# Performance work log

Measured on AMD Instinct MI355X. Metric: run time of the kernel, lower is better.

## Reference

```python
import jax, jax.numpy as jnp
import numpy as np

# Production-scale dims: N tokens = 64 batch x 8192 seq, hidden width 256.
N, D_IN, D_OUT = 524288, 256, 256
P_NONZERO = 0.05  # mimics bnn.random.calc_desired_var -> sparse ternary W


def binarise(v):
    # bnn.functions.binarise forward: sign with binarise(0) = +1
    return jnp.where(v >= 0, 1.0, -1.0).astype(v.dtype)


def setup_inputs() -> dict:
    key = jax.random.key(0)
    kx, kw = jax.random.split(key)
    # x: binary activations in {-1,+1} (output of a previous binarise layer)
    x = jnp.where(jax.random.normal(kx, (N, D_IN)) >= 0, 1.0, -1.0).astype(jnp.float32)
    # W: ternary {-1, 0, +1} with Var = P_NONZERO (values +-1 each w.p. p/2)
    u = jax.random.uniform(kw, (D_IN, D_OUT))
    W = jnp.where(u < P_NONZERO / 2, -1.0,
                  jnp.where(u < P_NONZERO, 1.0, 0.0)).astype(jnp.float32)
    return {"x": x, "W": W}


def reference(x, W):
    # integer = x @ W  (ternary-weight matmul; int math in torch, same values in fp32)
    integer = x @ W  # [N, D_OUT]
    return binarise(integer)
```

## Files before the change

kernel.cpp:

```cpp
#include <hip/hip_runtime.h>
#include <stdint.h>


#define NROWS 524288
#define DDIM  256
#define BLOCKS 2048
#define ROWS_PER_BLOCK (NROWS / BLOCKS)

typedef uint32_t u32;
typedef unsigned long long u64;

#define LOADG(v0, v1, v2, v3, ptr)                                   \
    v0 = *reinterpret_cast<const uint4*>(ptr);                       \
    v1 = *reinterpret_cast<const uint4*>((ptr) + DDIM);              \
    v2 = *reinterpret_cast<const uint4*>((ptr) + 2 * DDIM);          \
    v3 = *reinterpret_cast<const uint4*>((ptr) + 3 * DDIM);

#define PROC1(xv, optr)                                               \
    {                                                                 \
        const u64 _bl0 = __ballot((int)(xv).x < 0);                   \
        const u64 _bl1 = __ballot((int)(xv).y < 0);                   \
        const u64 _bl2 = __ballot((int)(xv).z < 0);                   \
        const u64 _bl3 = __ballot((int)(xv).w < 0);                   \
        int _p = 0;                                                   \
        _p += __popc(((u32)_bl0         ^ M0) & A0);                  \
        _p += __popc(((u32)(_bl0 >> 32) ^ M1) & A1);                  \
        _p += __popc(((u32)_bl1         ^ M2) & A2);                  \
        _p += __popc(((u32)(_bl1 >> 32) ^ M3) & A3);                  \
        _p += __popc(((u32)_bl2         ^ M4) & A4);                  \
        _p += __popc(((u32)(_bl2 >> 32) ^ M5) & A5);                  \
        _p += __popc(((u32)_bl3         ^ M6) & A6);                  \
        _p += __popc(((u32)(_bl3 >> 32) ^ M7) & A7);                  \
        const int _d = C - 2 * _p;                                    \
        const u32 _o = 0x3f800000u | ((u32)_d & 0x80000000u);         \
        __builtin_nontemporal_store(_o, reinterpret_cast<u32*>(optr));\
    }

#define PROC4(v0, v1, v2, v3, optr)                                  \
    PROC1(v0, (optr));                                               \
    PROC1(v1, (optr) + DDIM);                                        \
    PROC1(v2, (optr) + 2 * DDIM);                                    \
    PROC1(v3, (optr) + 3 * DDIM);

__global__ __launch_bounds__(256, 4)
void ternbin_kernel(const float* __restrict__ x, const float* __restrict__ W,
                    float* __restrict__ out) {
    const int t    = threadIdx.x;
    const int lane = t & 63;
    const int wv   = t >> 6;
    const int col  = (wv << 6) | lane;

    u32 A0=0,A1=0,A2=0,A3=0,A4=0,A5=0,A6=0,A7=0;
    u32 M0=0,M1=0,M2=0,M3=0,M4=0,M5=0,M6=0,M7=0;
    #pragma unroll 8
    for (int k = 0; k < DDIM; ++k) {
        const float v = W[k * DDIM + col];
        const int   w = ((k & 3) << 1) | (k >> 7);
        const u32 bit = 1u << ((k >> 2) & 31);
        const u32 nz  = (v != 0.0f) ? bit : 0u;
        const u32 ng  = (v <  0.0f) ? bit : 0u;
        switch (w) {
            case 0: A0 |= nz; M0 |= ng; break;
            case 1: A1 |= nz; M1 |= ng; break;
            case 2: A2 |= nz; M2 |= ng; break;
            case 3: A3 |= nz; M3 |= ng; break;
            case 4: A4 |= nz; M4 |= ng; break;
            case 5: A5 |= nz; M5 |= ng; break;
            case 6: A6 |= nz; M6 |= ng; break;
            case 7: A7 |= nz; M7 |= ng; break;
        }
    }
    const int C = __popc(A0) + __popc(A1) + __popc(A2) + __popc(A3)
                + __popc(A4) + __popc(A5) + __popc(A6) + __popc(A7);

    const size_t row0 = (size_t)blockIdx.x * ROWS_PER_BLOCK;
    const float* xq = x   + row0 * DDIM + 4 * lane;
    float*       oq = out + row0 * DDIM + col;

    uint4 a0, a1, a2, a3, b0, b1, b2, b3;
    LOADG(a0, a1, a2, a3, xq); xq += 4 * DDIM;
    LOADG(b0, b1, b2, b3, xq); xq += 4 * DDIM;
    __builtin_amdgcn_sched_barrier(0);

    #pragma unroll 1
    for (int k = 0; k < 31; ++k) {
        PROC4(a0, a1, a2, a3, oq); oq += 4 * DDIM;
        LOADG(a0, a1, a2, a3, xq); xq += 4 * DDIM;
        __builtin_amdgcn_sched_barrier(0);
        PROC4(b0, b1, b2, b3, oq); oq += 4 * DDIM;
        LOADG(b0, b1, b2, b3, xq); xq += 4 * DDIM;
        __builtin_amdgcn_sched_barrier(0);
    }
    PROC4(a0, a1, a2, a3, oq); oq += 4 * DDIM;
    PROC4(b0, b1, b2, b3, oq);
}

extern "C" void kernel_launch(void* const* d_in, const int* in_sizes, int n_in,
                              void* d_out, int out_size, void* d_ws, size_t ws_size,
                              hipStream_t stream) {
    const float* x = (const float*)d_in[0];
    const float* W = (const float*)d_in[1];
    float* out = (float*)d_out;
    ternbin_kernel<<<BLOCKS, 256, 0, stream>>>(x, W, out);
}
```

Baseline: 1.039 ms.

## Split sign packing and popcount into LDS-staged phases per block

Each block now runs in two phases. In the first, each wave loads its quarter of the rows, packs the sign bits with ballots and stores 8 words per row into shared memory, so each row's ballots are computed once instead of by all four waves. In the second, every thread reads the packed words from LDS and does the xor/popcount per output column. Launch bounds raise occupancy to 8 waves per SIMD. The cost is that the explicit double-buffered load/compute overlap is removed, a block barrier splits loads from stores, and LDS traffic is added.

```diff
diff --git a/kernel.cpp b/kernel.cpp
--- a/kernel.cpp
+++ b/kernel.cpp
@@ -2,49 +2,20 @@
 #include <stdint.h>
 
 
-#define NROWS 524288
-#define DDIM  256
+#define NROWS  524288
+#define DDIM   256
 #define BLOCKS 2048
-#define ROWS_PER_BLOCK (NROWS / BLOCKS)
+#define RPB    (NROWS / BLOCKS)
+#define RPW    (RPB / 4)
 
 typedef uint32_t u32;
 typedef unsigned long long u64;
 
-#define LOADG(v0, v1, v2, v3, ptr)                                   \
-    v0 = *reinterpret_cast<const uint4*>(ptr);                       \
-    v1 = *reinterpret_cast<const uint4*>((ptr) + DDIM);              \
-    v2 = *reinterpret_cast<const uint4*>((ptr) + 2 * DDIM);          \
-    v3 = *reinterpret_cast<const uint4*>((ptr) + 3 * DDIM);
-
-#define PROC1(xv, optr)                                               \
-    {                                                                 \
-        const u64 _bl0 = __ballot((int)(xv).x < 0);                   \
-        const u64 _bl1 = __ballot((int)(xv).y < 0);                   \
-        const u64 _bl2 = __ballot((int)(xv).z < 0);                   \
-        const u64 _bl3 = __ballot((int)(xv).w < 0);                   \
-        int _p = 0;                                                   \
-        _p += __popc(((u32)_bl0         ^ M0) & A0);                  \
-        _p += __popc(((u32)(_bl0 >> 32) ^ M1) & A1);                  \
-        _p += __popc(((u32)_bl1         ^ M2) & A2);                  \
-        _p += __popc(((u32)(_bl1 >> 32) ^ M3) & A3);                  \
-        _p += __popc(((u32)_bl2         ^ M4) & A4);                  \
-        _p += __popc(((u32)(_bl2 >> 32) ^ M5) & A5);                  \
-        _p += __popc(((u32)_bl3         ^ M6) & A6);                  \
-        _p += __popc(((u32)(_bl3 >> 32) ^ M7) & A7);                  \
-        const int _d = C - 2 * _p;                                    \
-        const u32 _o = 0x3f800000u | ((u32)_d & 0x80000000u);         \
-        __builtin_nontemporal_store(_o, reinterpret_cast<u32*>(optr));\
-    }
-
-#define PROC4(v0, v1, v2, v3, optr)                                  \
-    PROC1(v0, (optr));                                               \
-    PROC1(v1, (optr) + DDIM);                                        \
-    PROC1(v2, (optr) + 2 * DDIM);                                    \
-    PROC1(v3, (optr) + 3 * DDIM);
-
-__global__ __launch_bounds__(256, 4)
+__global__ __launch_bounds__(256, 8)
 void ternbin_kernel(const float* __restrict__ x, const float* __restrict__ W,
                     float* __restrict__ out) {
+    __shared__ u32 signs[RPB][8];
+
     const int t    = threadIdx.x;
     const int lane = t & 63;
     const int wv   = t >> 6;
@@ -73,26 +44,60 @@
     const int C = __popc(A0) + __popc(A1) + __popc(A2) + __popc(A3)
                 + __popc(A4) + __popc(A5) + __popc(A6) + __popc(A7);
 
-    const size_t row0 = (size_t)blockIdx.x * ROWS_PER_BLOCK;
-    const float* xq = x   + row0 * DDIM + 4 * lane;
-    float*       oq = out + row0 * DDIM + col;
+    const size_t row0 = (size_t)blockIdx.x * RPB;
 
-    uint4 a0, a1, a2, a3, b0, b1, b2, b3;
-    LOADG(a0, a1, a2, a3, xq); xq += 4 * DDIM;
-    LOADG(b0, b1, b2, b3, xq); xq += 4 * DDIM;
-    __builtin_amdgcn_sched_barrier(0);
+    {
+        const float* xp = x + (row0 + (size_t)wv * RPW) * DDIM + 4 * lane;
+        const bool writer  = (lane < 8);
+        const bool b2      = (lane & 4) != 0;
+        const bool b1      = (lane & 2) != 0;
+        const bool b0s     = (lane & 1) != 0;
 
-    #pragma unroll 1
-    for (int k = 0; k < 31; ++k) {
-        PROC4(a0, a1, a2, a3, oq); oq += 4 * DDIM;
-        LOADG(a0, a1, a2, a3, xq); xq += 4 * DDIM;
-        __builtin_amdgcn_sched_barrier(0);
-        PROC4(b0, b1, b2, b3, oq); oq += 4 * DDIM;
-        LOADG(b0, b1, b2, b3, xq); xq += 4 * DDIM;
-        __builtin_amdgcn_sched_barrier(0);
+        #pragma unroll 1
+        for (int r = 0; r < RPW; r += 4) {
+            uint4 v0 = *reinterpret_cast<const uint4*>(xp + (size_t)(r + 0) * DDIM);
+            uint4 v1 = *reinterpret_cast<const uint4*>(xp + (size_t)(r + 1) * DDIM);
+            uint4 v2 = *reinterpret_cast<const uint4*>(xp + (size_t)(r + 2) * DDIM);
+            uint4 v3 = *reinterpret_cast<const uint4*>(xp + (size_t)(r + 3) * DDIM);
+
+            #pragma unroll
+            for (int i = 0; i < 4; ++i) {
+                const uint4 v = (i == 0) ? v0 : (i == 1) ? v1 : (i == 2) ? v2 : v3;
+                const u64 q0 = __ballot((int)v.x < 0);
+                const u64 q1 = __ballot((int)v.y < 0);
+                const u64 q2 = __ballot((int)v.z < 0);
+                const u64 q3 = __ballot((int)v.w < 0);
+                const u32 w0 = (u32)q0, w1 = (u32)(q0 >> 32);
+                const u32 w2 = (u32)q1, w3 = (u32)(q1 >> 32);
+                const u32 w4 = (u32)q2, w5 = (u32)(q2 >> 32);
+                const u32 w6 = (u32)q3, w7 = (u32)(q3 >> 32);
+                const u32 sel = b2 ? (b1 ? (b0s ? w7 : w6) : (b0s ? w5 : w4))
+                                   : (b1 ? (b0s ? w3 : w2) : (b0s ? w1 : w0));
+                if (writer) signs[wv * RPW + r + i][lane] = sel;
+            }
+        }
     }
-    PROC4(a0, a1, a2, a3, oq); oq += 4 * DDIM;
-    PROC4(b0, b1, b2, b3, oq);
+    __syncthreads();
+
+    float* oq = out + row0 * DDIM + col;
+    #pragma unroll 2
+    for (int r = 0; r < RPB; ++r) {
+        const uint4 sa = *reinterpret_cast<const uint4*>(&signs[r][0]);
+        const uint4 sb = *reinterpret_cast<const uint4*>(&signs[r][4]);
+        int p = 0;
+        p += __popc((sa.x ^ M0) & A0);
+        p += __popc((sa.y ^ M1) & A1);
+        p += __popc((sa.z ^ M2) & A2);
+        p += __popc((sa.w ^ M3) & A3);
+        p += __popc((sb.x ^ M4) & A4);
+        p += __popc((sb.y ^ M5) & A5);
+        p += __popc((sb.z ^ M6) & A6);
+        p += __popc((sb.w ^ M7) & A7);
+        const int d = C - 2 * p;
+        const u32 o = 0x3f800000u | ((u32)d & 0x80000000u);
+        __builtin_nontemporal_store(o,
+            reinterpret_cast<u32*>(oq + (size_t)r * DDIM));
+    }
 }
 
 extern "C" void kernel_launch(void* const* d_in, const int* in_sizes, int n_in,
```

Result: faster. 982.9 us (-5.4%).
